# Kernel tuning notes

Measured on AMD Instinct MI355X. Metric: run time of the kernel, lower is better.

## Reference

```python
import jax, jax.numpy as jnp
import numpy as np

GAMMA = 0.99
GAE_LAMBDA = 0.95
CLIP_PARAM = 0.2
VALUE_LOSS_COEF = 0.5
ENTROPY_COEF = 0.01
T, N = 1024, 8192

def setup_inputs() -> dict:
    key = jax.random.key(0)
    ks = jax.random.split(key, 9)
    rewards = jax.random.normal(ks[0], (T, N, 1), dtype=jnp.float32)
    masks = (jax.random.uniform(ks[1], (T + 1, N, 1)) > 0.02).astype(jnp.float32)
    bad_masks = (jax.random.uniform(ks[2], (T + 1, N, 1)) > 0.01).astype(jnp.float32)
    value_preds = jax.random.normal(ks[3], (T + 1, N, 1), dtype=jnp.float32)
    last_value = jax.random.normal(ks[4], (N, 1), dtype=jnp.float32)
    log_prob = jax.random.normal(ks[5], (T, N, 1), dtype=jnp.float32) * 0.1
    prev_log_prob = jax.random.normal(ks[6], (T, N, 1), dtype=jnp.float32) * 0.1
    new_value = jax.random.normal(ks[7], (T, N, 1), dtype=jnp.float32)
    dist_entropy = jax.random.normal(ks[8], (T, N, 1), dtype=jnp.float32)
    return {"rewards": rewards, "masks": masks, "bad_masks": bad_masks,
            "value_preds": value_preds, "last_value": last_value,
            "log_prob": log_prob, "prev_log_prob": prev_log_prob,
            "new_value": new_value, "dist_entropy": dist_entropy}


def _compute_derived(rewards, masks, bad_masks, value_preds, last_value):
    # value_preds is detached in the original update(); mirror with stop_gradient
    vp = jax.lax.stop_gradient(value_preds)
    lv = jax.lax.stop_gradient(last_value)
    vp = vp.at[-1].set(lv)  # value_preds[-1] = last_value

    def step(gae, xs):
        r, v_next, v, m_next, bad_next = xs
        delta = r + GAMMA * v_next * m_next - v
        gae = (delta + GAMMA * GAE_LAMBDA * m_next * gae) * bad_next
        return gae, gae + v  # returns[step] = gae + value_preds[step]

    xs = (rewards, vp[1:], vp[:-1], masks[1:], bad_masks[1:])
    init = jnp.zeros_like(lv)
    _, returns_t = jax.lax.scan(step, init, xs, reverse=True)  # (T, N, 1)

    advantages = returns_t - vp[:-1]
    advantages = (advantages - advantages.mean()) / (advantages.std(ddof=1) + 1e-5)
    return advantages, returns_t


def reference(rewards, masks, bad_masks, value_preds, last_value,
              log_prob, prev_log_prob, new_value, dist_entropy):
    advantages, returns_t = _compute_derived(rewards, masks, bad_masks,
                                             value_preds, last_value)
    # PPO clipped surrogate (single minibatch = full rollout, flattened over T*N)
    ratio = jnp.exp(log_prob - prev_log_prob)
    surr1 = ratio * advantages
    surr2 = jnp.clip(ratio, 1.0 - CLIP_PARAM, 1.0 + CLIP_PARAM) * advantages
    action_loss = -jnp.minimum(surr1, surr2).mean()

    value_target = jax.lax.stop_gradient(returns_t)
    old_value = jax.lax.stop_gradient(value_preds[:-1])
    value_pred_clipped = old_value + jnp.clip(new_value - old_value,
                                              -CLIP_PARAM, CLIP_PARAM)
    value_losses = (new_value - value_target) ** 2
    value_losses_clipped = (value_pred_clipped - value_target) ** 2
    value_loss = 0.5 * jnp.maximum(value_losses, value_losses_clipped).mean()

    loss = (value_loss * VALUE_LOSS_COEF + action_loss
            - dist_entropy.mean() * ENTROPY_COEF)
    return loss
```

## Files before the change

kernel.cpp:

```cpp
#include <hip/hip_runtime.h>
#include <math.h>

#define T_DIM 1024
#define N_DIM 8192
#define M_TOT (T_DIM * N_DIM)
#define NV4   (N_DIM / 4)
#define L_CHUNK 8
#define C_CHUNKS (T_DIM / L_CHUNK)
#define PC_BLOCKS ((C_CHUNKS * NV4) / 256)
#define SCAN_BLOCKS ((NV4 * 32) / 256)

#define kGAMMA 0.99f
#define kGLAM  (0.99f * 0.95f)


__device__ __forceinline__ unsigned short f2bf(float f) {
    unsigned int u = __float_as_uint(f);
    u += 0x7fffu + ((u >> 16) & 1u);
    return (unsigned short)(u >> 16);
}
__device__ __forceinline__ float bf2f(unsigned short h) {
    return __uint_as_float(((unsigned int)h) << 16);
}

__global__ __launch_bounds__(256, 4) void k_pc(
    const float4* __restrict__ r4,
    const float4* __restrict__ m4,
    const float4* __restrict__ bm4,
    const float4* __restrict__ vp4,
    const float4* __restrict__ lv4,
    ushort4* __restrict__ b16,
    float4* __restrict__ A_out,
    float4* __restrict__ B_out)
{
    const int g  = blockIdx.x * 256 + threadIdx.x;
    const int j  = g & (NV4 - 1);
    const int c  = g >> 11;
    const int t0 = c * L_CHUNK;

    float4 vnext = (c == C_CHUNKS - 1) ? lv4[j] : vp4[(t0 + L_CHUNK) * NV4 + j];
    float4 Aa = make_float4(1.f, 1.f, 1.f, 1.f);
    float4 Bb = make_float4(0.f, 0.f, 0.f, 0.f);

    #pragma unroll
    for (int half = 0; half < 2; ++half) {
        const int ibase = (half == 0) ? 7 : 3;
        float4 R[4], V[4], M[4], BBv[4];
        #pragma unroll
        for (int u = 0; u < 4; ++u) {
            const int idx = (t0 + ibase - u) * NV4 + j;
            R[u]   = r4[idx];
            V[u]   = vp4[idx];
            M[u]   = m4[idx + NV4];
            BBv[u] = bm4[idx + NV4];
        }
        #pragma unroll
        for (int u = 0; u < 4; ++u) {
            ushort4 o;
#define P1C(comp) { \
            const float b = (fmaf(kGAMMA * M[u].comp, vnext.comp, R[u].comp) - V[u].comp) * BBv[u].comp; \
            const float a = kGLAM * M[u].comp * BBv[u].comp; \
            Aa.comp = a * Aa.comp; Bb.comp = fmaf(a, Bb.comp, b); \
            o.comp = (unsigned short)((f2bf(b) & 0xFFFEu) | ((M[u].comp * BBv[u].comp > 0.5f) ? 1u : 0u)); }
            P1C(x) P1C(y) P1C(z) P1C(w)
#undef P1C
            b16[(t0 + ibase - u) * NV4 + j] = o;
            vnext = V[u];
        }
    }
    A_out[c * NV4 + j] = Aa;
    B_out[c * NV4 + j] = Bb;
}

__global__ __launch_bounds__(256, 8) void k_scan(
    float4* __restrict__ Ag,
    const float4* __restrict__ Bg)
{
    const int u  = blockIdx.x * 256 + threadIdx.x;
    const int jj = u >> 5;
    const int k  = u & 31;

    float4 As[4], Bs[4];
    #pragma unroll
    for (int i = 0; i < 4; ++i) {
        As[i] = Ag[(4 * k + i) * NV4 + jj];
        Bs[i] = Bg[(4 * k + i) * NV4 + jj];
    }
    float4 Pa = As[3], Pb = Bs[3];
    #pragma unroll
    for (int i = 2; i >= 0; --i) {
        Pb.x = fmaf(As[i].x, Pb.x, Bs[i].x); Pa.x = As[i].x * Pa.x;
        Pb.y = fmaf(As[i].y, Pb.y, Bs[i].y); Pa.y = As[i].y * Pa.y;
        Pb.z = fmaf(As[i].z, Pb.z, Bs[i].z); Pa.z = As[i].z * Pa.z;
        Pb.w = fmaf(As[i].w, Pb.w, Bs[i].w); Pa.w = As[i].w * Pa.w;
    }
    #pragma unroll
    for (int d = 1; d < 32; d <<= 1) {
        const float nax = __shfl_down(Pa.x, d, 32), nay = __shfl_down(Pa.y, d, 32);
        const float naz = __shfl_down(Pa.z, d, 32), naw = __shfl_down(Pa.w, d, 32);
        const float nbx = __shfl_down(Pb.x, d, 32), nby = __shfl_down(Pb.y, d, 32);
        const float nbz = __shfl_down(Pb.z, d, 32), nbw = __shfl_down(Pb.w, d, 32);
        if (k + d < 32) {
            Pb.x = fmaf(Pa.x, nbx, Pb.x); Pa.x *= nax;
            Pb.y = fmaf(Pa.y, nby, Pb.y); Pa.y *= nay;
            Pb.z = fmaf(Pa.z, nbz, Pb.z); Pa.z *= naz;
            Pb.w = fmaf(Pa.w, nbw, Pb.w); Pa.w *= naw;
        }
    }
    float4 G;
    G.x = __shfl_down(Pb.x, 1, 32);
    G.y = __shfl_down(Pb.y, 1, 32);
    G.z = __shfl_down(Pb.z, 1, 32);
    G.w = __shfl_down(Pb.w, 1, 32);
    if (k == 31) G = make_float4(0.f, 0.f, 0.f, 0.f);
    #pragma unroll
    for (int i = 3; i >= 0; --i) {
        Ag[(4 * k + i) * NV4 + jj] = G;
        G.x = fmaf(As[i].x, G.x, Bs[i].x);
        G.y = fmaf(As[i].y, G.y, Bs[i].y);
        G.z = fmaf(As[i].z, G.z, Bs[i].z);
        G.w = fmaf(As[i].w, G.w, Bs[i].w);
    }
}

__global__ __launch_bounds__(256, 4) void k_gae(
    const ushort4* __restrict__ b16,
    const float4* __restrict__ g_in4,
    const float4* __restrict__ vp4,
    const float4* __restrict__ nv4,
    double* __restrict__ pg)
{
    const int g  = blockIdx.x * 256 + threadIdx.x;
    const int j  = g & (NV4 - 1);
    const int c  = g >> 11;
    const int t0 = c * L_CHUNK;

    float4 gae = g_in4[c * NV4 + j];
    float sg = 0.f, sg2 = 0.f, v_s = 0.f;

    ushort4 H[8]; float4 V[8], Q[8];
    #pragma unroll
    for (int u = 0; u < 8; ++u) {
        const int idx = (t0 + 7 - u) * NV4 + j;
        H[u] = b16[idx];
        V[u] = vp4[idx];
        Q[u] = nv4[idx];
    }
    #pragma unroll
    for (int u = 0; u < 8; ++u) {
#define P3C(comp, HH) { \
        const unsigned short h = (HH); \
        const float bf = bf2f(h); \
        const float a  = (h & 1u) ? kGLAM : 0.0f; \
        gae.comp = fmaf(a, gae.comp, bf); \
        sg += gae.comp; sg2 = fmaf(gae.comp, gae.comp, sg2); \
        const float qd = Q[u].comp - V[u].comp; \
        const float e1 = qd - gae.comp; \
        const float e2 = fminf(fmaxf(qd, -0.2f), 0.2f) - gae.comp; \
        v_s += fmaxf(e1 * e1, e2 * e2); }
        P3C(x, H[u].x) P3C(y, H[u].y) P3C(z, H[u].z) P3C(w, H[u].w)
#undef P3C
    }

    double d0 = (double)sg, d1 = (double)sg2, d2 = (double)v_s;
    #pragma unroll
    for (int off = 32; off > 0; off >>= 1) {
        d0 += __shfl_down(d0, off, 64);
        d1 += __shfl_down(d1, off, 64);
        d2 += __shfl_down(d2, off, 64);
    }
    __shared__ double sh[3][4];
    const int wid = threadIdx.x >> 6, lane = threadIdx.x & 63;
    if (lane == 0) { sh[0][wid] = d0; sh[1][wid] = d1; sh[2][wid] = d2; }
    __syncthreads();
    if (threadIdx.x == 0) {
        double t0s = 0, t1s = 0, t2s = 0;
        #pragma unroll
        for (int w = 0; w < 4; ++w) { t0s += sh[0][w]; t1s += sh[1][w]; t2s += sh[2][w]; }
        pg[blockIdx.x * 3 + 0] = t0s;
        pg[blockIdx.x * 3 + 1] = t1s;
        pg[blockIdx.x * 3 + 2] = t2s;
    }
}

__global__ __launch_bounds__(256) void k_stats(
    const double* __restrict__ pg, double* __restrict__ acc)
{
    double s0 = 0.0, s1 = 0.0, s2 = 0.0;
    for (int i = threadIdx.x; i < PC_BLOCKS; i += 256) {
        s0 += pg[i * 3 + 0];
        s1 += pg[i * 3 + 1];
        s2 += pg[i * 3 + 2];
    }
    #pragma unroll
    for (int off = 32; off > 0; off >>= 1) {
        s0 += __shfl_down(s0, off, 64);
        s1 += __shfl_down(s1, off, 64);
        s2 += __shfl_down(s2, off, 64);
    }
    __shared__ double sh[3][4];
    const int wid = threadIdx.x >> 6, lane = threadIdx.x & 63;
    if (lane == 0) { sh[0][wid] = s0; sh[1][wid] = s1; sh[2][wid] = s2; }
    __syncthreads();
    if (threadIdx.x == 0) {
        double sum = 0, sum2 = 0, vsum = 0;
        #pragma unroll
        for (int w = 0; w < 4; ++w) { sum += sh[0][w]; sum2 += sh[1][w]; vsum += sh[2][w]; }
        const double M = (double)M_TOT;
        const double mu = sum / M;
        double var = (sum2 - sum * sum / M) / (M - 1.0);
        if (var < 0.0) var = 0.0;
        acc[3] = vsum;
        acc[5] = mu;
        acc[6] = 1.0 / (sqrt(var) + 1e-5);
    }
}

__global__ __launch_bounds__(256, 4) void k_loss(
    const ushort4* __restrict__ b16,
    const float4* __restrict__ g_in4,
    const float4* __restrict__ lp4,
    const float4* __restrict__ plp4,
    const float4* __restrict__ ent4,
    const double* __restrict__ acc,
    double* __restrict__ pl)
{
    const int tid = threadIdx.x;
    const int g  = blockIdx.x * 256 + tid;
    const int j  = g & (NV4 - 1);
    const int c  = g >> 11;
    const int t0 = c * L_CHUNK;

    const float mu   = (float)acc[5];
    const float invs = (float)acc[6];

    float4 gv = g_in4[c * NV4 + j];
    float a_s = 0.f, e_s = 0.f;

    #pragma unroll
    for (int half = 0; half < 2; ++half) {
        const int ibase = (half == 0) ? 7 : 3;
        ushort4 H[4]; float4 L[4], P[4], E[4];
        #pragma unroll
        for (int u = 0; u < 4; ++u) {
            const int idx = (t0 + ibase - u) * NV4 + j;
            H[u] = b16[idx];
            L[u] = lp4[idx];
            P[u] = plp4[idx];
            E[u] = ent4[idx];
        }
        #pragma unroll
        for (int u = 0; u < 4; ++u) {
#define P5C(comp, HH) { \
            const unsigned short hh = (HH); \
            const float bf = bf2f(hh); \
            const float a  = (hh & 1u) ? kGLAM : 0.0f; \
            gv.comp = fmaf(a, gv.comp, bf); \
            const float x  = (gv.comp - mu) * invs; \
            const float rr = __expf(L[u].comp - P[u].comp); \
            const float rc = fminf(fmaxf(rr, 0.8f), 1.2f); \
            a_s += fminf(rr * x, rc * x); }
            P5C(x, H[u].x) P5C(y, H[u].y) P5C(z, H[u].z) P5C(w, H[u].w)
#undef P5C
            e_s += E[u].x + E[u].y + E[u].z + E[u].w;
        }
    }

    double d0 = (double)a_s, d1 = (double)e_s;
    #pragma unroll
    for (int off = 32; off > 0; off >>= 1) {
        d0 += __shfl_down(d0, off, 64);
        d1 += __shfl_down(d1, off, 64);
    }
    __shared__ double sh[2][4];
    const int wid = tid >> 6, lane = tid & 63;
    if (lane == 0) { sh[0][wid] = d0; sh[1][wid] = d1; }
    __syncthreads();
    if (tid == 0) {
        double t0s = 0, t1s = 0;
        #pragma unroll
        for (int w = 0; w < 4; ++w) { t0s += sh[0][w]; t1s += sh[1][w]; }
        pl[blockIdx.x * 2 + 0] = t0s;
        pl[blockIdx.x * 2 + 1] = t1s;
    }
}

__global__ __launch_bounds__(256) void k_final(
    const double* __restrict__ pl, const double* __restrict__ acc,
    float* __restrict__ out)
{
    double s0 = 0.0, s1 = 0.0;
    for (int i = threadIdx.x; i < PC_BLOCKS; i += 256) {
        s0 += pl[i * 2 + 0];
        s1 += pl[i * 2 + 1];
    }
    #pragma unroll
    for (int off = 32; off > 0; off >>= 1) {
        s0 += __shfl_down(s0, off, 64);
        s1 += __shfl_down(s1, off, 64);
    }
    __shared__ double sh[2][4];
    const int wid = threadIdx.x >> 6, lane = threadIdx.x & 63;
    if (lane == 0) { sh[0][wid] = s0; sh[1][wid] = s1; }
    __syncthreads();
    if (threadIdx.x == 0) {
        double a_sum = 0, e_sum = 0;
        #pragma unroll
        for (int w = 0; w < 4; ++w) { a_sum += sh[0][w]; e_sum += sh[1][w]; }
        const double M = (double)M_TOT;
        out[0] = (float)(0.25 * acc[3] / M - a_sum / M - 0.01 * e_sum / M);
    }
}

extern "C" void kernel_launch(void* const* d_in, const int* in_sizes, int n_in,
                              void* d_out, int out_size, void* d_ws, size_t ws_size,
                              hipStream_t stream) {
    const float* rewards     = (const float*)d_in[0];
    const float* masks       = (const float*)d_in[1];
    const float* bad_masks   = (const float*)d_in[2];
    const float* value_preds = (const float*)d_in[3];
    const float* last_value  = (const float*)d_in[4];
    const float* log_prob    = (const float*)d_in[5];
    const float* prev_lp     = (const float*)d_in[6];
    const float* new_value   = (const float*)d_in[7];
    const float* dist_ent    = (const float*)d_in[8];

    char* ws = (char*)d_ws;
    double* acc = (double*)ws;
    double* pg  = (double*)(ws + 256);
    double* pl  = (double*)(ws + 32768);
    unsigned short* b16 = (unsigned short*)(ws + 65536);
    float* A = (float*)(ws + 65536 + (size_t)M_TOT * 2);
    float* B = (float*)(ws + 65536 + (size_t)M_TOT * 2 + (size_t)C_CHUNKS * N_DIM * 4);

    k_pc<<<PC_BLOCKS, 256, 0, stream>>>((const float4*)rewards,
                                        (const float4*)masks,
                                        (const float4*)bad_masks,
                                        (const float4*)value_preds,
                                        (const float4*)last_value,
                                        (ushort4*)b16, (float4*)A, (float4*)B);
    k_scan<<<SCAN_BLOCKS, 256, 0, stream>>>((float4*)A, (const float4*)B);
    k_gae<<<PC_BLOCKS, 256, 0, stream>>>((const ushort4*)b16,
                                         (const float4*)A ,
                                         (const float4*)value_preds,
                                         (const float4*)new_value, pg);
    k_stats<<<1, 256, 0, stream>>>(pg, acc);
    k_loss<<<PC_BLOCKS, 256, 0, stream>>>((const ushort4*)b16,
                                          (const float4*)A ,
                                          (const float4*)log_prob,
                                          (const float4*)prev_lp,
                                          (const float4*)dist_ent, acc, pl);
    k_final<<<1, 256, 0, stream>>>(pl, acc, (float*)d_out);
}
```

Measured before the change: 272.5 us.

## Precompute bf16 value delta in first pass and fold reductions via atomics

The first pass now also reads new_value and stores (new_value - value_pred) as a bf16 array, so the GAE pass reads two 16-bit streams instead of two fp32 arrays. The separate stats and final reduction kernels are removed. Per-block partial sums are atomically added into double accumulators, and the last-arriving block (tracked by a counter) computes the statistics and the final loss. This cuts GAE-pass traffic and two kernel launches, but it adds bf16 rounding to the value-loss term and makes the summation order nondeterministic.

Result: slower. 363.7 us (+33.5%).

```diff
diff --git a/kernel.cpp b/kernel.cpp
--- a/kernel.cpp
+++ b/kernel.cpp
@@ -23,17 +23,25 @@
     return __uint_as_float(((unsigned int)h) << 16);
 }
 
-__global__ __launch_bounds__(256, 4) void k_pc(
+__global__ __launch_bounds__(256) void k_pc(
     const float4* __restrict__ r4,
     const float4* __restrict__ m4,
     const float4* __restrict__ bm4,
     const float4* __restrict__ vp4,
     const float4* __restrict__ lv4,
+    const float4* __restrict__ nv4,
     ushort4* __restrict__ b16,
+    ushort4* __restrict__ q16,
     float4* __restrict__ A_out,
-    float4* __restrict__ B_out)
+    float4* __restrict__ B_out,
+    double* __restrict__ acc,
+    unsigned int* __restrict__ cnt)
 {
     const int g  = blockIdx.x * 256 + threadIdx.x;
+    if (g == 0) {
+        acc[1] = 0.0; acc[2] = 0.0; acc[3] = 0.0; acc[7] = 0.0; acc[8] = 0.0;
+        cnt[0] = 0u; cnt[1] = 0u;
+    }
     const int j  = g & (NV4 - 1);
     const int c  = g >> 11;
     const int t0 = c * L_CHUNK;
@@ -43,30 +51,26 @@
     float4 Bb = make_float4(0.f, 0.f, 0.f, 0.f);
 
     #pragma unroll
-    for (int half = 0; half < 2; ++half) {
-        const int ibase = (half == 0) ? 7 : 3;
-        float4 R[4], V[4], M[4], BBv[4];
-        #pragma unroll
-        for (int u = 0; u < 4; ++u) {
-            const int idx = (t0 + ibase - u) * NV4 + j;
-            R[u]   = r4[idx];
-            V[u]   = vp4[idx];
-            M[u]   = m4[idx + NV4];
-            BBv[u] = bm4[idx + NV4];
-        }
-        #pragma unroll
-        for (int u = 0; u < 4; ++u) {
-            ushort4 o;
+    for (int i = L_CHUNK - 1; i >= 0; --i) {
+        const int idx = (t0 + i) * NV4 + j;
+        const float4 r  = r4[idx];
+        const float4 v  = vp4[idx];
+        const float4 nv = nv4[idx];
+        const float4 m  = m4[idx + NV4];
+        const float4 bb = bm4[idx + NV4];
+
+        ushort4 o, qo;
 #define P1C(comp) { \
-            const float b = (fmaf(kGAMMA * M[u].comp, vnext.comp, R[u].comp) - V[u].comp) * BBv[u].comp; \
-            const float a = kGLAM * M[u].comp * BBv[u].comp; \
-            Aa.comp = a * Aa.comp; Bb.comp = fmaf(a, Bb.comp, b); \
-            o.comp = (unsigned short)((f2bf(b) & 0xFFFEu) | ((M[u].comp * BBv[u].comp > 0.5f) ? 1u : 0u)); }
-            P1C(x) P1C(y) P1C(z) P1C(w)
+        const float b = (fmaf(kGAMMA * m.comp, vnext.comp, r.comp) - v.comp) * bb.comp; \
+        const float a = kGLAM * m.comp * bb.comp; \
+        Aa.comp = a * Aa.comp; Bb.comp = fmaf(a, Bb.comp, b); \
+        o.comp  = (unsigned short)((f2bf(b) & 0xFFFEu) | ((m.comp * bb.comp > 0.5f) ? 1u : 0u)); \
+        qo.comp = f2bf(nv.comp - v.comp); }
+        P1C(x) P1C(y) P1C(z) P1C(w)
 #undef P1C
-            b16[(t0 + ibase - u) * NV4 + j] = o;
-            vnext = V[u];
-        }
+        b16[idx] = o;
+        q16[idx] = qo;
+        vnext = v;
     }
     A_out[c * NV4 + j] = Aa;
     B_out[c * NV4 + j] = Bb;
@@ -123,12 +127,12 @@
     }
 }
 
-__global__ __launch_bounds__(256, 4) void k_gae(
+__global__ __launch_bounds__(256) void k_gae(
     const ushort4* __restrict__ b16,
+    const ushort4* __restrict__ q16,
     const float4* __restrict__ g_in4,
-    const float4* __restrict__ vp4,
-    const float4* __restrict__ nv4,
-    double* __restrict__ pg)
+    double* __restrict__ acc,
+    unsigned int* __restrict__ cnt)
 {
     const int g  = blockIdx.x * 256 + threadIdx.x;
     const int j  = g & (NV4 - 1);
@@ -138,27 +142,22 @@
     float4 gae = g_in4[c * NV4 + j];
     float sg = 0.f, sg2 = 0.f, v_s = 0.f;
 
-    ushort4 H[8]; float4 V[8], Q[8];
-    #pragma unroll
-    for (int u = 0; u < 8; ++u) {
-        const int idx = (t0 + 7 - u) * NV4 + j;
-        H[u] = b16[idx];
-        V[u] = vp4[idx];
-        Q[u] = nv4[idx];
-    }
-    #pragma unroll
-    for (int u = 0; u < 8; ++u) {
-#define P3C(comp, HH) { \
-        const unsigned short h = (HH); \
-        const float bf = bf2f(h); \
-        const float a  = (h & 1u) ? kGLAM : 0.0f; \
+    #pragma unroll
+    for (int i = L_CHUNK - 1; i >= 0; --i) {
+        const int idx = (t0 + i) * NV4 + j;
+        const ushort4 h = b16[idx];
+        const ushort4 qh = q16[idx];
+#define P3C(comp, HH, QH) { \
+        const unsigned short hh = (HH); \
+        const float bf = bf2f(hh); \
+        const float a  = (hh & 1u) ? kGLAM : 0.0f; \
         gae.comp = fmaf(a, gae.comp, bf); \
         sg += gae.comp; sg2 = fmaf(gae.comp, gae.comp, sg2); \
-        const float qd = Q[u].comp - V[u].comp; \
+        const float qd = bf2f(QH); \
         const float e1 = qd - gae.comp; \
         const float e2 = fminf(fmaxf(qd, -0.2f), 0.2f) - gae.comp; \
         v_s += fmaxf(e1 * e1, e2 * e2); }
-        P3C(x, H[u].x) P3C(y, H[u].y) P3C(z, H[u].z) P3C(w, H[u].w)
+        P3C(x, h.x, qh.x) P3C(y, h.y, qh.y) P3C(z, h.z, qh.z) P3C(w, h.w, qh.w)
 #undef P3C
     }
 
@@ -177,42 +176,21 @@
         double t0s = 0, t1s = 0, t2s = 0;
         #pragma unroll
         for (int w = 0; w < 4; ++w) { t0s += sh[0][w]; t1s += sh[1][w]; t2s += sh[2][w]; }
-        pg[blockIdx.x * 3 + 0] = t0s;
-        pg[blockIdx.x * 3 + 1] = t1s;
-        pg[blockIdx.x * 3 + 2] = t2s;
-    }
-}
-
-__global__ __launch_bounds__(256) void k_stats(
-    const double* __restrict__ pg, double* __restrict__ acc)
-{
-    double s0 = 0.0, s1 = 0.0, s2 = 0.0;
-    for (int i = threadIdx.x; i < PC_BLOCKS; i += 256) {
-        s0 += pg[i * 3 + 0];
-        s1 += pg[i * 3 + 1];
-        s2 += pg[i * 3 + 2];
-    }
-    #pragma unroll
-    for (int off = 32; off > 0; off >>= 1) {
-        s0 += __shfl_down(s0, off, 64);
-        s1 += __shfl_down(s1, off, 64);
-        s2 += __shfl_down(s2, off, 64);
-    }
-    __shared__ double sh[3][4];
-    const int wid = threadIdx.x >> 6, lane = threadIdx.x & 63;
-    if (lane == 0) { sh[0][wid] = s0; sh[1][wid] = s1; sh[2][wid] = s2; }
-    __syncthreads();
-    if (threadIdx.x == 0) {
-        double sum = 0, sum2 = 0, vsum = 0;
-        #pragma unroll
-        for (int w = 0; w < 4; ++w) { sum += sh[0][w]; sum2 += sh[1][w]; vsum += sh[2][w]; }
-        const double M = (double)M_TOT;
-        const double mu = sum / M;
-        double var = (sum2 - sum * sum / M) / (M - 1.0);
-        if (var < 0.0) var = 0.0;
-        acc[3] = vsum;
-        acc[5] = mu;
-        acc[6] = 1.0 / (sqrt(var) + 1e-5);
+        atomicAdd(&acc[1], t0s);
+        atomicAdd(&acc[2], t1s);
+        atomicAdd(&acc[3], t2s);
+        __threadfence();
+        const unsigned int old = atomicAdd(&cnt[0], 1u);
+        if (old == (unsigned int)(PC_BLOCKS - 1)) {
+            __threadfence();
+            const double M = (double)M_TOT;
+            const double sum = acc[1], sum2 = acc[2];
+            const double mu = sum / M;
+            double var = (sum2 - sum * sum / M) / (M - 1.0);
+            if (var < 0.0) var = 0.0;
+            acc[5] = mu;
+            acc[6] = 1.0 / (sqrt(var) + 1e-5);
+        }
     }
 }
 
@@ -222,8 +200,9 @@
     const float4* __restrict__ lp4,
     const float4* __restrict__ plp4,
     const float4* __restrict__ ent4,
-    const double* __restrict__ acc,
-    double* __restrict__ pl)
+    double* __restrict__ acc,
+    unsigned int* __restrict__ cnt,
+    float* __restrict__ out)
 {
     const int tid = threadIdx.x;
     const int g  = blockIdx.x * 256 + tid;
@@ -280,35 +259,15 @@
         double t0s = 0, t1s = 0;
         #pragma unroll
         for (int w = 0; w < 4; ++w) { t0s += sh[0][w]; t1s += sh[1][w]; }
-        pl[blockIdx.x * 2 + 0] = t0s;
-        pl[blockIdx.x * 2 + 1] = t1s;
-    }
-}
-
-__global__ __launch_bounds__(256) void k_final(
-    const double* __restrict__ pl, const double* __restrict__ acc,
-    float* __restrict__ out)
-{
-    double s0 = 0.0, s1 = 0.0;
-    for (int i = threadIdx.x; i < PC_BLOCKS; i += 256) {
-        s0 += pl[i * 2 + 0];
-        s1 += pl[i * 2 + 1];
-    }
-    #pragma unroll
-    for (int off = 32; off > 0; off >>= 1) {
-        s0 += __shfl_down(s0, off, 64);
-        s1 += __shfl_down(s1, off, 64);
-    }
-    __shared__ double sh[2][4];
-    const int wid = threadIdx.x >> 6, lane = threadIdx.x & 63;
-    if (lane == 0) { sh[0][wid] = s0; sh[1][wid] = s1; }
-    __syncthreads();
-    if (threadIdx.x == 0) {
-        double a_sum = 0, e_sum = 0;
-        #pragma unroll
-        for (int w = 0; w < 4; ++w) { a_sum += sh[0][w]; e_sum += sh[1][w]; }
-        const double M = (double)M_TOT;
-        out[0] = (float)(0.25 * acc[3] / M - a_sum / M - 0.01 * e_sum / M);
+        atomicAdd(&acc[7], t0s);
+        atomicAdd(&acc[8], t1s);
+        __threadfence();
+        const unsigned int old = atomicAdd(&cnt[1], 1u);
+        if (old == (unsigned int)(PC_BLOCKS - 1)) {
+            __threadfence();
+            const double M = (double)M_TOT;
+            out[0] = (float)(0.25 * acc[3] / M - acc[7] / M - 0.01 * acc[8] / M);
+        }
     }
 }
 
@@ -327,28 +286,29 @@
 
     char* ws = (char*)d_ws;
     double* acc = (double*)ws;
-    double* pg  = (double*)(ws + 256);
-    double* pl  = (double*)(ws + 32768);
+    unsigned int* cnt = (unsigned int*)(ws + 128);
     unsigned short* b16 = (unsigned short*)(ws + 65536);
-    float* A = (float*)(ws + 65536 + (size_t)M_TOT * 2);
-    float* B = (float*)(ws + 65536 + (size_t)M_TOT * 2 + (size_t)C_CHUNKS * N_DIM * 4);
+    unsigned short* q16 = (unsigned short*)(ws + 65536 + (size_t)M_TOT * 2);
+    float* A = (float*)(ws + 65536 + (size_t)M_TOT * 4);
+    float* B = (float*)(ws + 65536 + (size_t)M_TOT * 4 + (size_t)C_CHUNKS * N_DIM * 4);
 
     k_pc<<<PC_BLOCKS, 256, 0, stream>>>((const float4*)rewards,
                                         (const float4*)masks,
                                         (const float4*)bad_masks,
                                         (const float4*)value_preds,
                                         (const float4*)last_value,
-                                        (ushort4*)b16, (float4*)A, (float4*)B);
+                                        (const float4*)new_value,
+                                        (ushort4*)b16, (ushort4*)q16,
+                                        (float4*)A, (float4*)B, acc, cnt);
     k_scan<<<SCAN_BLOCKS, 256, 0, stream>>>((float4*)A, (const float4*)B);
     k_gae<<<PC_BLOCKS, 256, 0, stream>>>((const ushort4*)b16,
+                                         (const ushort4*)q16,
                                          (const float4*)A ,
-                                         (const float4*)value_preds,
-                                         (const float4*)new_value, pg);
-    k_stats<<<1, 256, 0, stream>>>(pg, acc);
+                                         acc, cnt);
     k_loss<<<PC_BLOCKS, 256, 0, stream>>>((const ushort4*)b16,
                                           (const float4*)A ,
                                           (const float4*)log_prob,
                                           (const float4*)prev_lp,
-                                          (const float4*)dist_ent, acc, pl);
-    k_final<<<1, 256, 0, stream>>>(pl, acc, (float*)d_out);
-}
+                                          (const float4*)dist_ent,
+                                          acc, cnt, (float*)d_out);
+}
```
